# Kernel tuning notes

Hardware: AMD Instinct MI355X
Metric: run time of the kernel (lower is better)

Reference implementation:

```python
import jax, jax.numpy as jnp
import numpy as np

B, D, N, S = 4096, 768, 8192, 4  # batch, embedding_dim, len(y)==cat rows, source_size


def setup_inputs() -> dict:
    key = jax.random.key(0)
    k1, k2, k3, k4 = jax.random.split(key, 4)
    batch_x = jax.random.normal(k1, (B, D), dtype=jnp.float32)
    cat = jax.random.normal(k2, (N, D), dtype=jnp.float32)
    y = jax.random.randint(k3, (N,), 0, 2, dtype=jnp.int32)
    # phi_srcs: xavier-uniform-like scale for (D, 1) params, stacked as [S, D]
    phi = jax.random.normal(k4, (S, D), dtype=jnp.float32) * 0.05
    bias = jnp.zeros((1,), dtype=jnp.float32)
    return {"batch_x": batch_x, "cat": cat, "y": y, "phi": phi, "bias": bias}


def reference(batch_x, cat, y, phi, bias):
    # con[n, b] = cat[n] . batch_x[b]   -> [N, B]
    con = jnp.einsum('nd,bd->nb', cat, batch_x)
    # F.normalize(con, p=4, dim=0): divide each column by its 4-norm (eps=1e-12)
    norm4 = jnp.power(jnp.sum(jnp.abs(con) ** 4, axis=0), 0.25)
    con = con / jnp.maximum(norm4, 1e-12)
    # softmax over all N rows (dim=0), per batch column
    con = jax.nn.softmax(con, axis=0)
    # chunk into S sources along the N axis: psi [S, N/S, B]
    psi = con.reshape(S, N // S, B)
    yf = y.astype(jnp.float32).reshape(S, N // S)  # y chunks [S, N/S]
    # theta_s = exp(x @ phi_s): [S, B]  (unnormalized, as in the original output path)
    theta = jnp.exp(jnp.einsum('bd,sd->sb', batch_x, phi))
    # per-source: sum_n y[s,n] * psi[s,n,b], then scale by theta[s,b]; sum over sources
    sum_matrix = jnp.sum(jnp.einsum('sn,snb->sb', yf, psi) * theta, axis=0)  # [B]
    y_hat = jax.nn.sigmoid(sum_matrix + bias)  # bias [1] broadcasts -> [B]
    return y_hat
```

## Files before the change

kernel.cpp:

```cpp
#include <hip/hip_runtime.h>
#include <hip/hip_bf16.h>
#include <stdint.h>
#include <math.h>

#define Bdim 4096
#define Ddim 768
#define Ndim 8192
#define Sdim 4

typedef __attribute__((ext_vector_type(4))) float floatx4;
typedef __attribute__((ext_vector_type(8))) int int8v;
typedef __attribute__((ext_vector_type(4))) int int4v;

__device__ inline int pack_fp8x4(float4 v) {
  int r = __builtin_amdgcn_cvt_pk_fp8_f32(v.x, v.y, 0, 0);
  r = __builtin_amdgcn_cvt_pk_fp8_f32(v.z, v.w, r, 1);
  return r;
}

__device__ __forceinline__ void gl_lds16(const void* g, void* lds_base) {
  __builtin_amdgcn_global_load_lds(
      (const __attribute__((address_space(1))) unsigned int*)g,
      (__attribute__((address_space(3))) unsigned int*)lds_base, 16, 0, 0);
}

__global__ void convert_kernel(const float* __restrict__ x,
                               const float* __restrict__ cat,
                               const float* __restrict__ phi,
                               unsigned char* __restrict__ xq,
                               unsigned char* __restrict__ catq,
                               float* __restrict__ stats,
                               float* __restrict__ theta) {
  int gid = blockIdx.x * blockDim.x + threadIdx.x;
  int stride = gridDim.x * blockDim.x;
  const int nx4 = (Bdim * Ddim) / 4;
  const int nc4 = (Ndim * Ddim) / 4;
  for (int i = gid; i < nx4; i += stride)
    ((int*)xq)[i] = pack_fp8x4(((const float4*)x)[i]);
  for (int i = gid; i < nc4; i += stride)
    ((int*)catq)[i] = pack_fp8x4(((const float4*)cat)[i]);
  if (gid < 6 * Bdim) stats[gid] = 0.0f;

  int gw = gid >> 6;
  int lane = threadIdx.x & 63;
  if (gw < Bdim) {
    const float4* xr4 = (const float4*)(x + (size_t)gw * Ddim);
    const float4* ph4 = (const float4*)phi;
    const int D4 = Ddim / 4;
    float a0 = 0.f, a1 = 0.f, a2 = 0.f, a3 = 0.f;
#pragma unroll
    for (int d4 = lane; d4 < D4; d4 += 64) {
      float4 xv = xr4[d4];
      float4 p0 = ph4[d4];
      float4 p1 = ph4[D4 + d4];
      float4 p2 = ph4[2 * D4 + d4];
      float4 p3 = ph4[3 * D4 + d4];
      a0 = fmaf(xv.x, p0.x, fmaf(xv.y, p0.y, fmaf(xv.z, p0.z, fmaf(xv.w, p0.w, a0))));
      a1 = fmaf(xv.x, p1.x, fmaf(xv.y, p1.y, fmaf(xv.z, p1.z, fmaf(xv.w, p1.w, a1))));
      a2 = fmaf(xv.x, p2.x, fmaf(xv.y, p2.y, fmaf(xv.z, p2.z, fmaf(xv.w, p2.w, a2))));
      a3 = fmaf(xv.x, p3.x, fmaf(xv.y, p3.y, fmaf(xv.z, p3.z, fmaf(xv.w, p3.w, a3))));
    }
#pragma unroll
    for (int off = 32; off > 0; off >>= 1) {
      a0 += __shfl_down(a0, off);
      a1 += __shfl_down(a1, off);
      a2 += __shfl_down(a2, off);
      a3 += __shfl_down(a3, off);
    }
    if (lane == 0) {
      theta[gw] = __expf(a0);
      theta[Bdim + gw] = __expf(a1);
      theta[2 * Bdim + gw] = __expf(a2);
      theta[3 * Bdim + gw] = __expf(a3);
    }
  }
}

__global__ __launch_bounds__(256, 4) void gemm_bt_kernel(
    const unsigned char* __restrict__ A,
    const unsigned char* __restrict__ Bm,
    unsigned int* __restrict__ Cw,
    float* __restrict__ s4) {
  __shared__ unsigned char As[128 * 128];
  __shared__ unsigned char Bs[128 * 128];

  const int tid = threadIdx.x;
  const int wave = tid >> 6;
  const int lane = tid & 63;
  const int quad = lane >> 4;
  const int l16 = lane & 15;
  const int wm = (wave & 1) * 64;
  const int wn = (wave >> 1) * 64;
  const int m0 = blockIdx.x * 128;
  const int n0 = blockIdx.y * 128;

  floatx4 acc[4][4];
#pragma unroll
  for (int i = 0; i < 4; ++i)
#pragma unroll
    for (int j = 0; j < 4; ++j) acc[i][j] = (floatx4){0.f, 0.f, 0.f, 0.f};

  const unsigned char* a_src[4];
  const unsigned char* b_src[4];
#pragma unroll
  for (int i = 0; i < 4; ++i) {
    int p = tid + 256 * i;
    int row = ((p >> 6) << 3) + (p & 7);
    int colb = ((p >> 3) & 7) * 16;
    a_src[i] = A + (size_t)(m0 + row) * Ddim + colb;
    b_src[i] = Bm + (size_t)(n0 + row) * Ddim + colb;
  }
  const int wbase = (wave * 64) * 16;

#pragma unroll
  for (int i = 0; i < 4; ++i) {
    gl_lds16(a_src[i], &As[wbase + i * 4096]);
    gl_lds16(b_src[i], &Bs[wbase + i * 4096]);
  }
  __syncthreads();

  for (int kk = 0; kk < 6; ++kk) {
    int8v af[4], bf[4];
#pragma unroll
    for (int mi = 0; mi < 4; ++mi) {
      int r = wm + mi * 16 + l16;
      int base = ((r >> 3) << 10) + quad * 256 + (r & 7) * 16;
      int4v lo = *(const int4v*)(&As[base]);
      int4v hi = *(const int4v*)(&As[base + 128]);
      af[mi] = __builtin_shufflevector(lo, hi, 0, 1, 2, 3, 4, 5, 6, 7);
    }
#pragma unroll
    for (int ni = 0; ni < 4; ++ni) {
      int r = wn + ni * 16 + l16;
      int base = ((r >> 3) << 10) + quad * 256 + (r & 7) * 16;
      int4v lo = *(const int4v*)(&Bs[base]);
      int4v hi = *(const int4v*)(&Bs[base + 128]);
      bf[ni] = __builtin_shufflevector(lo, hi, 0, 1, 2, 3, 4, 5, 6, 7);
    }
#pragma unroll
    for (int mi = 0; mi < 4; ++mi)
#pragma unroll
      for (int ni = 0; ni < 4; ++ni)
        acc[mi][ni] = __builtin_amdgcn_mfma_scale_f32_16x16x128_f8f6f4(
            af[mi], bf[ni], acc[mi][ni], 0, 0,
            0, 0x7f7f7f7f,
            0, 0x7f7f7f7f);

    __syncthreads();

    if (kk < 5) {
      const int k0 = (kk + 1) * 128;
#pragma unroll
      for (int i = 0; i < 4; ++i) {
        gl_lds16(a_src[i] + k0, &As[wbase + i * 4096]);
        gl_lds16(b_src[i] + k0, &Bs[wbase + i * 4096]);
      }
      __syncthreads();
    }
  }

  float cs4[4] = {0.f, 0.f, 0.f, 0.f};
#pragma unroll
  for (int mi = 0; mi < 4; ++mi)
#pragma unroll
    for (int ni = 0; ni < 4; ++ni) {
      int g = (m0 + wm + mi * 16) / 4 + quad;
      int col = n0 + wn + ni * 16 + l16;
      floatx4 a = acc[mi][ni];
      int w = __builtin_amdgcn_cvt_pk_fp8_f32(a[0], a[1], 0, 0);
      w = __builtin_amdgcn_cvt_pk_fp8_f32(a[2], a[3], w, 1);
      Cw[(size_t)g * Bdim + col] = (unsigned int)w;
#pragma unroll
      for (int rr = 0; rr < 4; ++rr) {
        float c2 = a[rr] * a[rr];
        cs4[ni] += c2 * c2;
      }
    }
#pragma unroll
  for (int ni = 0; ni < 4; ++ni) {
    float v = cs4[ni];
    v += __shfl_xor(v, 16);
    v += __shfl_xor(v, 32);
    if (quad == 0) atomicAdd(&s4[n0 + wn + ni * 16 + l16], v);
  }
}

__global__ void expsum_kernel(const unsigned int* __restrict__ conq,
                              const float* __restrict__ s4,
                              const int* __restrict__ y,
                              float* __restrict__ denom,
                              float* __restrict__ numer) {
  int b = blockIdx.x * 256 + threadIdx.x;
  int g0 = blockIdx.y * 16;
  int src = (g0 * 4) / (Ndim / Sdim);

  float inv = 1.0f / fmaxf(sqrtf(sqrtf(s4[b])), 1e-12f);
  float inv2 = inv * 1.4426950408889634f;
  const unsigned int* p = conq + (size_t)g0 * Bdim + b;
  float dsum = 0.f, nsum = 0.f;
#pragma unroll 4
  for (int i = 0; i < 16; ++i) {
    unsigned int w = p[(size_t)i * Bdim];
    int4 yv = *(const int4*)(y + 4 * (g0 + i));
    float e0 = exp2f(__builtin_amdgcn_cvt_f32_fp8(w, 0) * inv2);
    float e1 = exp2f(__builtin_amdgcn_cvt_f32_fp8(w, 1) * inv2);
    float e2 = exp2f(__builtin_amdgcn_cvt_f32_fp8(w, 2) * inv2);
    float e3 = exp2f(__builtin_amdgcn_cvt_f32_fp8(w, 3) * inv2);
    dsum += e0 + e1 + e2 + e3;
    nsum += e0 * (float)yv.x + e1 * (float)yv.y + e2 * (float)yv.z +
            e3 * (float)yv.w;
  }
  atomicAdd(&denom[b], dsum);
  atomicAdd(&numer[src * Bdim + b], nsum);
}

__global__ void finalize_kernel(const float* __restrict__ denom,
                                const float* __restrict__ numer,
                                const float* __restrict__ theta,
                                const float* __restrict__ bias,
                                float* __restrict__ out) {
  int b = blockIdx.x * 256 + threadIdx.x;
  float acc = 0.f;
#pragma unroll
  for (int si = 0; si < Sdim; ++si)
    acc += numer[si * Bdim + b] * theta[si * Bdim + b];
  float z = acc / denom[b] + bias[0];
  out[b] = 1.0f / (1.0f + __expf(-z));
}

extern "C" void kernel_launch(void* const* d_in, const int* in_sizes, int n_in,
                              void* d_out, int out_size, void* d_ws,
                              size_t ws_size, hipStream_t stream) {
  const float* batch_x = (const float*)d_in[0];
  const float* cat = (const float*)d_in[1];
  const int* y = (const int*)d_in[2];
  const float* phi = (const float*)d_in[3];
  const float* bias = (const float*)d_in[4];
  float* out = (float*)d_out;

  char* ws = (char*)d_ws;
  unsigned char* catq = (unsigned char*)ws;
  unsigned char* xq = catq + (size_t)Ndim * Ddim;
  unsigned int* conq = (unsigned int*)(xq + (size_t)Bdim * Ddim);
  float* stats = (float*)((unsigned char*)conq + (size_t)Ndim * Bdim);
  float* s4 = stats;
  float* denom = s4 + Bdim;
  float* numer = denom + Bdim;
  float* theta = stats + 6 * Bdim;

  convert_kernel<<<2048, 256, 0, stream>>>(batch_x, cat, phi, xq, catq, stats,
                                           theta);

  dim3 g2(Ndim / 128, Bdim / 128);
  gemm_bt_kernel<<<g2, 256, 0, stream>>>(catq, xq, conq, s4);

  dim3 g3(Bdim / 256, 128);
  expsum_kernel<<<g3, 256, 0, stream>>>(conq, s4, y, denom, numer);

  finalize_kernel<<<Bdim / 256, 256, 0, stream>>>(denom, numer, theta, bias,
                                                  out);
}
```

Measured before the change: 175.1 us.

## Prefetch next K tile into registers during MFMA instead of direct global-to-LDS loads

Replaces the global_load_lds direct-to-LDS copies with ordinary global loads into registers. The loads for the next K tile are issued before the current tile's MFMAs and written to LDS after the barrier, so global latency overlaps compute instead of stalling between iterations. It also drops the occupancy hint of 4 from launch_bounds. The cost is extra VGPRs for the staging registers and explicit LDS stores, which may reduce occupancy.

```diff
diff --git a/kernel.cpp b/kernel.cpp
--- a/kernel.cpp
+++ b/kernel.cpp
@@ -16,12 +16,6 @@
   int r = __builtin_amdgcn_cvt_pk_fp8_f32(v.x, v.y, 0, 0);
   r = __builtin_amdgcn_cvt_pk_fp8_f32(v.z, v.w, r, 1);
   return r;
-}
-
-__device__ __forceinline__ void gl_lds16(const void* g, void* lds_base) {
-  __builtin_amdgcn_global_load_lds(
-      (const __attribute__((address_space(1))) unsigned int*)g,
-      (__attribute__((address_space(3))) unsigned int*)lds_base, 16, 0, 0);
 }
 
 __global__ void convert_kernel(const float* __restrict__ x,
@@ -76,7 +70,7 @@
   }
 }
 
-__global__ __launch_bounds__(256, 4) void gemm_bt_kernel(
+__global__ __launch_bounds__(256) void gemm_bt_kernel(
     const unsigned char* __restrict__ A,
     const unsigned char* __restrict__ Bm,
     unsigned int* __restrict__ Cw,
@@ -110,31 +104,45 @@
     a_src[i] = A + (size_t)(m0 + row) * Ddim + colb;
     b_src[i] = Bm + (size_t)(n0 + row) * Ddim + colb;
   }
-  const int wbase = (wave * 64) * 16;
-
+
+  int4v areg[4], breg[4];
 #pragma unroll
   for (int i = 0; i < 4; ++i) {
-    gl_lds16(a_src[i], &As[wbase + i * 4096]);
-    gl_lds16(b_src[i], &Bs[wbase + i * 4096]);
+    areg[i] = *(const int4v*)(a_src[i]);
+    breg[i] = *(const int4v*)(b_src[i]);
+  }
+#pragma unroll
+  for (int i = 0; i < 4; ++i) {
+    *(int4v*)(As + (tid + 256 * i) * 16) = areg[i];
+    *(int4v*)(Bs + (tid + 256 * i) * 16) = breg[i];
   }
   __syncthreads();
 
   for (int kk = 0; kk < 6; ++kk) {
+    if (kk < 5) {
+      const int k0 = (kk + 1) * 128;
+#pragma unroll
+      for (int i = 0; i < 4; ++i) {
+        areg[i] = *(const int4v*)(a_src[i] + k0);
+        breg[i] = *(const int4v*)(b_src[i] + k0);
+      }
+    }
+
     int8v af[4], bf[4];
 #pragma unroll
     for (int mi = 0; mi < 4; ++mi) {
       int r = wm + mi * 16 + l16;
       int base = ((r >> 3) << 10) + quad * 256 + (r & 7) * 16;
-      int4v lo = *(const int4v*)(&As[base]);
-      int4v hi = *(const int4v*)(&As[base + 128]);
+      int4v lo = *(const int4v*)(As + base);
+      int4v hi = *(const int4v*)(As + base + 128);
       af[mi] = __builtin_shufflevector(lo, hi, 0, 1, 2, 3, 4, 5, 6, 7);
     }
 #pragma unroll
     for (int ni = 0; ni < 4; ++ni) {
       int r = wn + ni * 16 + l16;
       int base = ((r >> 3) << 10) + quad * 256 + (r & 7) * 16;
-      int4v lo = *(const int4v*)(&Bs[base]);
-      int4v hi = *(const int4v*)(&Bs[base + 128]);
+      int4v lo = *(const int4v*)(Bs + base);
+      int4v hi = *(const int4v*)(Bs + base + 128);
       bf[ni] = __builtin_shufflevector(lo, hi, 0, 1, 2, 3, 4, 5, 6, 7);
     }
 #pragma unroll
@@ -149,11 +157,10 @@
     __syncthreads();
 
     if (kk < 5) {
-      const int k0 = (kk + 1) * 128;
 #pragma unroll
       for (int i = 0; i < 4; ++i) {
-        gl_lds16(a_src[i] + k0, &As[wbase + i * 4096]);
-        gl_lds16(b_src[i] + k0, &Bs[wbase + i * 4096]);
+        *(int4v*)(As + (tid + 256 * i) * 16) = areg[i];
+        *(int4v*)(Bs + (tid + 256 * i) * 16) = breg[i];
       }
       __syncthreads();
     }
```

Result: faster. 156.7 us (-10.5%).
